# Optimization experiments

Measured on AMD Instinct MI355X. Metric: run time of the kernel, lower is better.

Reference implementation:

```python
import jax, jax.numpy as jnp
import numpy as np
from jax import lax

SIGMA = 1.0          # block_elemnts.combined_sigma
BN_EPS = 1e-5


def setup_inputs() -> dict:
    key = jax.random.key(0)
    k1, k2, k3, k4 = jax.random.split(key, 4)
    B, N, T, C_in, C_out = 8, 1024, 8, 64, 64
    return {
        "points": jax.random.normal(k1, (B, N, 3), dtype=jnp.float32),
        "translations": jax.random.normal(k2, (B, T, 3), dtype=jnp.float32),
        "functions": jax.random.normal(k3, (B, N, C_in), dtype=jnp.float32),
        "k_tensor": jax.random.normal(k4, (C_out, C_in, T), dtype=jnp.float32)
            * np.sqrt(2.0 / (C_in + C_out)),  # xavier_normal_
        "gamma": jnp.ones((C_out,), dtype=jnp.float32),
        "beta": jnp.zeros((C_out,), dtype=jnp.float32),
    }


def reference(points, translations, functions, k_tensor, gamma, beta):
    denom = 2.0 * SIGMA ** 2
    # pairwise squared distances [B,N,N]
    sq = jnp.sum(points * points, axis=-1)                      # [B,N]
    dist = sq[:, :, None] + sq[:, None, :] \
        - 2.0 * jnp.einsum('bnd,bmd->bnm', points, points)      # [B,N,N]
    # interpolation matrix = Gaussian kernel of distances
    interp_rowsum = jnp.sum(jnp.exp(-dist / denom), axis=2, keepdims=True)  # [B,N,1]
    w = functions / interp_rowsum                               # [B,N,Cin]
    # b_tensor[t] = w @ k_tensor[:,:,t]^T  -> [T,B,N,Cout]
    b = jnp.einsum('bnc,oct->tbno', w, k_tensor)
    ptd = jnp.einsum('bnd,btd->tbn', points, translations)      # [T,B,N]
    tsq = jnp.sum(translations * translations, axis=2).T        # [T,B]

    B_, N_, O_ = b.shape[1], b.shape[2], b.shape[3]

    def step(acc, inputs):
        b_t, ptd_t, tsq_t = inputs                              # [B,N,O],[B,N],[B]
        dot = -2.0 * ptd_t                                      # [B,N]
        # exponent = -||p_i - p_j - t||^2 / (2*sigma^2), always <= 0
        q = jnp.exp(-(dist + dot[:, :, None] - dot[:, None, :]
                      + tsq_t[:, None, None]) / denom)          # [B,N,N]
        return acc + jnp.einsum('bnm,bmo->bno', q, b_t), None

    out, _ = lax.scan(step, jnp.zeros((B_, N_, O_), dtype=b.dtype),
                      (b, ptd, tsq))                            # [B,N,O]

    # BatchNorm1d in training mode over (B,N) per channel, then ReLU
    mean = jnp.mean(out, axis=(0, 1))
    var = jnp.var(out, axis=(0, 1))
    xn = (out - mean) * lax.rsqrt(var + BN_EPS) * gamma + beta
    return jax.nn.relu(xn)                                      # [B,N,Cout]
```

## Files before the change

kernel.cpp:

```cpp
#include <hip/hip_runtime.h>
#include <hip/hip_bf16.h>
#include <cstdint>
#include <cstddef>

#define BN_EPS 1e-5f

typedef float f32x4_t __attribute__((ext_vector_type(4)));
typedef __bf16 bf16x8_t __attribute__((ext_vector_type(8)));

__device__ __forceinline__ unsigned short f2bf(float f) {
    __hip_bfloat16 h = __float2bfloat16(f);
    return __builtin_bit_cast(unsigned short, h);
}
__device__ __forceinline__ float bf2f(unsigned short u) {
    unsigned int v = ((unsigned int)u) << 16;
    return __builtin_bit_cast(float, v);
}

__device__ __forceinline__ void gld_lds16(void* lds, const void* gp) {
#if __has_builtin(__builtin_amdgcn_global_load_lds)
    __builtin_amdgcn_global_load_lds(
        (const __attribute__((address_space(1))) unsigned int*)gp,
        (__attribute__((address_space(3))) unsigned int*)lds, 16, 0, 0);
#else
    *(uint4*)lds = *(const uint4*)gp;
#endif
}


__global__ __launch_bounds__(256) void k_g(const float* __restrict__ points,
                                           const float* __restrict__ ktens,
                                           unsigned short* __restrict__ G,
                                           float* __restrict__ rowsum,
                                           unsigned short* __restrict__ kpb,
                                           float* __restrict__ bns) {
    __shared__ float praw[3072];
    __shared__ float px[1024], py[1024], pz[1024], hq[1024];
    __shared__ float part[8][128];
    __shared__ float p2[8][32];

    const int tid = threadIdx.x;
    if (blockIdx.x >= 1024) {
        const int i = (blockIdx.x - 1024) * 256 + tid;
        const int t = i >> 12, o = (i >> 6) & 63, c = i & 63;
        kpb[i] = f2bf(ktens[(o * 64 + c) * 8 + t]);
        if (blockIdx.x == 1024 && tid < 128) bns[tid] = 0.f;
        return;
    }

    const int b  = blockIdx.x & 7;
    const int n0 = (blockIdx.x >> 3) * 8;

    for (int i = tid; i < 3072; i += 256) praw[i] = points[b * 3072 + i];
    __syncthreads();
    for (int n = tid; n < 1024; n += 256) {
        float x = praw[n * 3], y = praw[n * 3 + 1], z = praw[n * 3 + 2];
        px[n] = x; py[n] = y; pz[n] = z;
        hq[n] = -0.5f * (x * x + y * y + z * z);
    }
    __syncthreads();

    const int rhalf = tid >> 7;
    const int c0 = (tid & 127) * 8;
    float vx[8], vy[8], vz[8], vh[8];
    *(float4*)&vx[0] = *(const float4*)&px[c0];
    *(float4*)&vx[4] = *(const float4*)&px[c0 + 4];
    *(float4*)&vy[0] = *(const float4*)&py[c0];
    *(float4*)&vy[4] = *(const float4*)&py[c0 + 4];
    *(float4*)&vz[0] = *(const float4*)&pz[c0];
    *(float4*)&vz[4] = *(const float4*)&pz[c0 + 4];
    *(float4*)&vh[0] = *(const float4*)&hq[c0];
    *(float4*)&vh[4] = *(const float4*)&hq[c0 + 4];

    unsigned short* gb = G + ((size_t)b << 20);

    #pragma unroll
    for (int u = 0; u < 4; ++u) {
        const int rl = u * 2 + rhalf;
        const int row = n0 + rl;
        const float rx = px[row], ry = py[row], rz = pz[row], hr = hq[row];
        unsigned short us[8];
        float ssum = 0.f;
        #pragma unroll
        for (int j = 0; j < 8; ++j) {
            float e = __expf(hr + vh[j] + rx * vx[j] + ry * vy[j] + rz * vz[j]);
            ssum += e;
            us[j] = f2bf(e);
        }
        uint4 pk;
        pk.x = us[0] | ((unsigned int)us[1] << 16);
        pk.y = us[2] | ((unsigned int)us[3] << 16);
        pk.z = us[4] | ((unsigned int)us[5] << 16);
        pk.w = us[6] | ((unsigned int)us[7] << 16);
        *(uint4*)(gb + (size_t)row * 1024 + c0) = pk;
        part[rl][tid & 127] = ssum;
    }
    __syncthreads();
    {
        const int row = tid >> 5, c4l = (tid & 31) * 4;
        float4 p = *(const float4*)&part[row][c4l];
        p2[row][tid & 31] = p.x + p.y + p.z + p.w;
    }
    __syncthreads();
    if (tid < 8) {
        float s = 0.f;
        #pragma unroll
        for (int q = 0; q < 8; ++q) {
            float4 v = *(const float4*)&p2[tid][q * 4];
            s += v.x + v.y + v.z + v.w;
        }
        rowsum[b * 1024 + n0 + tid] = s;
    }
}

__global__ __launch_bounds__(256) void k_prep(const float* __restrict__ points,
                                              const float* __restrict__ trans,
                                              const float* __restrict__ funcs,
                                              const unsigned short* __restrict__ kpb,
                                              const float* __restrict__ rowsum,
                                              unsigned short* __restrict__ bmatT,
                                              float* __restrict__ escale) {
    __shared__ unsigned short Asm[128 * 72];
    __shared__ unsigned short Bsm[128 * 72];
    __shared__ float sfacl[256];

    const int b  = blockIdx.x & 7;
    const int mt = (blockIdx.x >> 3) & 7;
    const int ct = blockIdx.x >> 6;
    const int m0 = mt * 128;

    const int tid  = threadIdx.x;
    const int wave = tid >> 6, lane = tid & 63;
    const int wr = wave >> 1, wc = wave & 1;
    const int fr = lane & 15, quad = lane >> 4;

    {
        const int tloc = tid >> 7, m = tid & 127;
        const int t = ct * 2 + tloc;
        const float tx = trans[b * 24 + t * 3], ty = trans[b * 24 + t * 3 + 1],
                    tz = trans[b * 24 + t * 3 + 2];
        const float* pp = &points[(size_t)(b * 1024 + m0 + m) * 3];
        const float ptd = pp[0] * tx + pp[1] * ty + pp[2] * tz;
        const float tsq = tx * tx + ty * ty + tz * tz;
        const float rsv = rowsum[b * 1024 + m0 + m];
        sfacl[tloc * 128 + m] = __expf(-ptd - 0.5f * tsq) / rsv;
        escale[(size_t)(b * 8 + t) * 1024 + m0 + m] = __expf(ptd);
    }
    #pragma unroll
    for (int rep = 0; rep < 2; ++rep) {
        const int m = rep * 64 + (tid >> 2);
        const int c16 = (tid & 3) * 16;
        const float* fp = &funcs[((size_t)(b * 1024) + m0 + m) * 64 + c16];
        float4 f0 = *(const float4*)fp, f1 = *(const float4*)(fp + 4);
        float4 f2 = *(const float4*)(fp + 8), f3 = *(const float4*)(fp + 12);
        uint4 p0, p1;
        p0.x = f2bf(f0.x) | ((unsigned)f2bf(f0.y) << 16);
        p0.y = f2bf(f0.z) | ((unsigned)f2bf(f0.w) << 16);
        p0.z = f2bf(f1.x) | ((unsigned)f2bf(f1.y) << 16);
        p0.w = f2bf(f1.z) | ((unsigned)f2bf(f1.w) << 16);
        p1.x = f2bf(f2.x) | ((unsigned)f2bf(f2.y) << 16);
        p1.y = f2bf(f2.z) | ((unsigned)f2bf(f2.w) << 16);
        p1.z = f2bf(f3.x) | ((unsigned)f2bf(f3.y) << 16);
        p1.w = f2bf(f3.z) | ((unsigned)f2bf(f3.w) << 16);
        *(uint4*)&Asm[m * 72 + c16] = p0;
        *(uint4*)&Asm[m * 72 + c16 + 8] = p1;
    }
    #pragma unroll
    for (int rep = 0; rep < 4; ++rep) {
        const int col = rep * 32 + (tid >> 3);
        const int c8 = (tid & 7) * 8;
        uint4 v = *(const uint4*)&kpb[(size_t)(ct * 128 + col) * 64 + c8];
        *(uint4*)&Bsm[col * 72 + c8] = v;
    }
    __syncthreads();

    f32x4_t acc[4][4];
    #pragma unroll
    for (int i = 0; i < 4; ++i)
        #pragma unroll
        for (int j = 0; j < 4; ++j) acc[i][j] = f32x4_t{0.f, 0.f, 0.f, 0.f};

    #pragma unroll
    for (int s = 0; s < 2; ++s) {
        uint4 afr[4], bfr[4];
        #pragma unroll
        for (int i = 0; i < 4; ++i)
            afr[i] = *(const uint4*)&Asm[(wr * 64 + i * 16 + fr) * 72 + s * 32 + quad * 8];
        #pragma unroll
        for (int j = 0; j < 4; ++j)
            bfr[j] = *(const uint4*)&Bsm[(wc * 64 + j * 16 + fr) * 72 + s * 32 + quad * 8];
        #pragma unroll
        for (int i = 0; i < 4; ++i)
            #pragma unroll
            for (int j = 0; j < 4; ++j)
                acc[i][j] = __builtin_amdgcn_mfma_f32_16x16x32_bf16(
                    __builtin_bit_cast(bf16x8_t, afr[i]),
                    __builtin_bit_cast(bf16x8_t, bfr[j]),
                    acc[i][j], 0, 0, 0);
    }

    #pragma unroll
    for (int i = 0; i < 4; ++i) {
        #pragma unroll
        for (int j = 0; j < 4; ++j) {
            const int colg = ct * 128 + wc * 64 + j * 16 + fr;
            ushort4 pk;
            {
                const int mb = wr * 64 + i * 16 + quad * 4;
                pk.x = f2bf(acc[i][j][0] * sfacl[wc * 128 + mb + 0]);
                pk.y = f2bf(acc[i][j][1] * sfacl[wc * 128 + mb + 1]);
                pk.z = f2bf(acc[i][j][2] * sfacl[wc * 128 + mb + 2]);
                pk.w = f2bf(acc[i][j][3] * sfacl[wc * 128 + mb + 3]);
                *(ushort4*)&bmatT[(size_t)(b * 512 + colg) * 1024 + m0 + mb] = pk;
            }
        }
    }
}

__global__ __launch_bounds__(256) void k_gemm(const unsigned short* __restrict__ G,
                                              const unsigned short* __restrict__ bmatT,
                                              const float* __restrict__ escale,
                                              unsigned short* __restrict__ He2) {
    __shared__ unsigned short As[4096];
    __shared__ unsigned short Bs[4096];
    __shared__ float escT[1024];

    const int b  = blockIdx.x & 7;
    const int rt = (blockIdx.x >> 3) & 7;
    const int z  = blockIdx.x >> 6;
    const int og = z & 3;
    const int kh = z >> 2;
    const int n0 = rt * 128;
    const int kb = kh * 256;

    const int tid  = threadIdx.x;
    const int wave = tid >> 6, lane = tid & 63;

    {
        const int t = tid >> 5, r4 = (tid & 31) * 4;
        *(float4*)&escT[t * 128 + r4] =
            *(const float4*)&escale[(size_t)(b * 8 + t) * 1024 + n0 + r4];
    }

    const unsigned short* gA = G + ((size_t)b << 20) + (size_t)n0 * 1024 + kb;
    const unsigned short* gB = bmatT + (size_t)(b * 512 + og * 16) * 1024 + kb;

    const int r16 = lane >> 2;
    const int kq  = lane & 3;
    const int gsw = kq ^ (r16 & 3);
    const size_t gAoff = (size_t)r16 * 1024 + gsw * 8;

    f32x4_t acc[2][8];
    #pragma unroll
    for (int i = 0; i < 2; ++i)
        #pragma unroll
        for (int j = 0; j < 8; ++j) acc[i][j] = f32x4_t{0.f, 0.f, 0.f, 0.f};

    const int fr = lane & 15;
    const int swoff = ((lane >> 4) ^ (fr & 3)) << 4;
    const int row_base = wave * 32;

    for (int kk = 0; kk < 8; ++kk) {
        const int k0 = kk * 32;
        __syncthreads();
        #pragma unroll
        for (int i = 0; i < 2; ++i) {
            const int seg = wave * 2 + i;
            gld_lds16((char*)As + seg * 1024 + lane * 16,
                      gA + (size_t)(seg * 16) * 1024 + k0 + gAoff);
            gld_lds16((char*)Bs + seg * 1024 + lane * 16,
                      gB + (size_t)(seg * 64) * 1024 + (size_t)r16 * 1024 + k0 + gsw * 8);
        }
        __syncthreads();
        uint4 afr0 = *(const uint4*)((const char*)As + (row_base + fr) * 64 + swoff);
        uint4 afr1 = *(const uint4*)((const char*)As + (row_base + 16 + fr) * 64 + swoff);
        #pragma unroll
        for (int j = 0; j < 8; ++j) {
            uint4 bfr = *(const uint4*)((const char*)Bs + (j * 16 + fr) * 64 + swoff);
            acc[0][j] = __builtin_amdgcn_mfma_f32_16x16x32_bf16(
                __builtin_bit_cast(bf16x8_t, afr0),
                __builtin_bit_cast(bf16x8_t, bfr), acc[0][j], 0, 0, 0);
            acc[1][j] = __builtin_amdgcn_mfma_f32_16x16x32_bf16(
                __builtin_bit_cast(bf16x8_t, afr1),
                __builtin_bit_cast(bf16x8_t, bfr), acc[1][j], 0, 0, 0);
        }
    }

    const int quad = lane >> 4, oo = lane & 15;
    unsigned short* dst = He2 + (size_t)kh * 524288
                              + (size_t)(b * 1024 + n0) * 64 + og * 16;
    #pragma unroll
    for (int i = 0; i < 2; ++i) {
        #pragma unroll
        for (int r = 0; r < 4; ++r) {
            const int row = row_base + i * 16 + quad * 4 + r;
            float s = 0.f;
            #pragma unroll
            for (int j = 0; j < 8; ++j)
                s += escT[j * 128 + row] * acc[i][j][r];
            dst[(size_t)row * 64 + oo] = f2bf(s);
        }
    }
}

__global__ __launch_bounds__(256) void k_fin(const unsigned short* __restrict__ He2,
                                             float* __restrict__ out,
                                             float* __restrict__ bns) {
    __shared__ float s1[16][64], s2[16][64];
    const int tid = threadIdx.x;
    float a0 = 0.f, a1 = 0.f, a2 = 0.f, a3 = 0.f;
    float q0 = 0.f, q1 = 0.f, q2 = 0.f, q3 = 0.f;
    #pragma unroll
    for (int it = 0; it < 2; ++it) {
        const size_t idx = (size_t)blockIdx.x * 512 + it * 256 + tid;
        float4 s = make_float4(0.f, 0.f, 0.f, 0.f);
        #pragma unroll
        for (int p = 0; p < 4; ++p) {
            ushort4 u = *(const ushort4*)(He2 + (size_t)p * 524288 + idx * 4);
            s.x += bf2f(u.x); s.y += bf2f(u.y); s.z += bf2f(u.z); s.w += bf2f(u.w);
        }
        ((float4*)out)[idx] = s;
        a0 += s.x; a1 += s.y; a2 += s.z; a3 += s.w;
        q0 += s.x * s.x; q1 += s.y * s.y; q2 += s.z * s.z; q3 += s.w * s.w;
    }
    const int g = tid >> 4, o4 = (tid & 15) * 4;
    *(float4*)&s1[g][o4] = make_float4(a0, a1, a2, a3);
    *(float4*)&s2[g][o4] = make_float4(q0, q1, q2, q3);
    __syncthreads();
    if (tid < 64) {
        float sa = 0.f, sb = 0.f;
        #pragma unroll
        for (int r = 0; r < 16; ++r) { sa += s1[r][tid]; sb += s2[r][tid]; }
        atomicAdd(&bns[tid], sa);
        atomicAdd(&bns[64 + tid], sb);
    }
}

__global__ __launch_bounds__(256) void k_bn(float* __restrict__ out,
                                            const float* __restrict__ bns,
                                            const float* __restrict__ gamma,
                                            const float* __restrict__ beta) {
    const int i = blockIdx.x * 256 + threadIdx.x;
    const int o4 = (i & 15) * 4;
    float4 x = ((float4*)out)[i];
    const float4 s  = *(const float4*)&bns[o4];
    const float4 s2 = *(const float4*)&bns[64 + o4];
    const float4 gm = *(const float4*)&gamma[o4];
    const float4 bt = *(const float4*)&beta[o4];
    const float invn = 1.f / 8192.f;
    float m, v, w;
    m = s.x * invn; v = s2.x * invn - m * m; w = __frsqrt_rn(v + BN_EPS) * gm.x;
    x.x = fmaxf((x.x - m) * w + bt.x, 0.f);
    m = s.y * invn; v = s2.y * invn - m * m; w = __frsqrt_rn(v + BN_EPS) * gm.y;
    x.y = fmaxf((x.y - m) * w + bt.y, 0.f);
    m = s.z * invn; v = s2.z * invn - m * m; w = __frsqrt_rn(v + BN_EPS) * gm.z;
    x.z = fmaxf((x.z - m) * w + bt.z, 0.f);
    m = s.w * invn; v = s2.w * invn - m * m; w = __frsqrt_rn(v + BN_EPS) * gm.w;
    x.w = fmaxf((x.w - m) * w + bt.w, 0.f);
    ((float4*)out)[i] = x;
}

extern "C" void kernel_launch(void* const* d_in, const int* in_sizes, int n_in,
                              void* d_out, int out_size, void* d_ws, size_t ws_size,
                              hipStream_t stream) {
    const float* points = (const float*)d_in[0];
    const float* trans  = (const float*)d_in[1];
    const float* funcs  = (const float*)d_in[2];
    const float* ktens  = (const float*)d_in[3];
    const float* gamma  = (const float*)d_in[4];
    const float* beta   = (const float*)d_in[5];
    float* out = (float*)d_out;

    float* ws      = (float*)d_ws;
    float* escale  = ws;
    float* bns     = escale + 65536;
    float* rowsum  = bns + 128;
    unsigned short* He2   = (unsigned short*)(rowsum + 8192);
    unsigned short* kpb   = He2 + 2097152;
    unsigned short* G     = kpb + 32768;
    unsigned short* bmatT = G + 8388608;

    k_g<<<1152, 256, 0, stream>>>(points, ktens, G, rowsum, kpb, bns);
    k_prep<<<256, 256, 0, stream>>>(points, trans, funcs, kpb, rowsum, bmatT, escale);
    k_gemm<<<1024, 256, 0, stream>>>(G, bmatT, escale, He2);
    k_fin<<<256, 256, 0, stream>>>(He2, out, bns);
    k_bn<<<512, 256, 0, stream>>>(out, bns, gamma, beta);
}
```

Measured before the change: 115.3 us.

## Recompute Gaussian matrix tiles inside GEMM instead of materializing G

The 16 MB bf16 Gaussian matrix G is no longer written by k_g. k_gemm now regenerates the A-operand fragments in registers from point coordinates staged in LDS, computing exp per element before each MFMA step. This removes the global write and re-read of G across the 4 output groups. The cost is more exp work, since each G tile is recomputed by every output-group and k-half block (4x redundancy), and those exps now sit on the MFMA critical path.

```diff
diff --git a/kernel.cpp b/kernel.cpp
--- a/kernel.cpp
+++ b/kernel.cpp
@@ -30,7 +30,6 @@
 
 __global__ __launch_bounds__(256) void k_g(const float* __restrict__ points,
                                            const float* __restrict__ ktens,
-                                           unsigned short* __restrict__ G,
                                            float* __restrict__ rowsum,
                                            unsigned short* __restrict__ kpb,
                                            float* __restrict__ bns) {
@@ -72,27 +71,15 @@
     *(float4*)&vh[0] = *(const float4*)&hq[c0];
     *(float4*)&vh[4] = *(const float4*)&hq[c0 + 4];
 
-    unsigned short* gb = G + ((size_t)b << 20);
-
     #pragma unroll
     for (int u = 0; u < 4; ++u) {
         const int rl = u * 2 + rhalf;
         const int row = n0 + rl;
         const float rx = px[row], ry = py[row], rz = pz[row], hr = hq[row];
-        unsigned short us[8];
         float ssum = 0.f;
         #pragma unroll
-        for (int j = 0; j < 8; ++j) {
-            float e = __expf(hr + vh[j] + rx * vx[j] + ry * vy[j] + rz * vz[j]);
-            ssum += e;
-            us[j] = f2bf(e);
-        }
-        uint4 pk;
-        pk.x = us[0] | ((unsigned int)us[1] << 16);
-        pk.y = us[2] | ((unsigned int)us[3] << 16);
-        pk.z = us[4] | ((unsigned int)us[5] << 16);
-        pk.w = us[6] | ((unsigned int)us[7] << 16);
-        *(uint4*)(gb + (size_t)row * 1024 + c0) = pk;
+        for (int j = 0; j < 8; ++j)
+            ssum += __expf(hr + vh[j] + rx * vx[j] + ry * vy[j] + rz * vz[j]);
         part[rl][tid & 127] = ssum;
     }
     __syncthreads();
@@ -217,13 +204,13 @@
     }
 }
 
-__global__ __launch_bounds__(256) void k_gemm(const unsigned short* __restrict__ G,
+__global__ __launch_bounds__(256) void k_gemm(const float* __restrict__ points,
                                               const unsigned short* __restrict__ bmatT,
                                               const float* __restrict__ escale,
                                               unsigned short* __restrict__ He2) {
-    __shared__ unsigned short As[4096];
     __shared__ unsigned short Bs[4096];
     __shared__ float escT[1024];
+    __shared__ float4 mp[256];
 
     const int b  = blockIdx.x & 7;
     const int rt = (blockIdx.x >> 3) & 7;
@@ -241,24 +228,38 @@
         *(float4*)&escT[t * 128 + r4] =
             *(const float4*)&escale[(size_t)(b * 8 + t) * 1024 + n0 + r4];
     }
-
-    const unsigned short* gA = G + ((size_t)b << 20) + (size_t)n0 * 1024 + kb;
+    {
+        const float* pp = &points[(size_t)(b * 1024 + kb + tid) * 3];
+        const float x = pp[0], y = pp[1], zz = pp[2];
+        mp[tid] = make_float4(x, y, zz, -0.5f * (x * x + y * y + zz * zz));
+    }
+
     const unsigned short* gB = bmatT + (size_t)(b * 512 + og * 16) * 1024 + kb;
 
     const int r16 = lane >> 2;
     const int kq  = lane & 3;
     const int gsw = kq ^ (r16 & 3);
-    const size_t gAoff = (size_t)r16 * 1024 + gsw * 8;
+
+    const int fr = lane & 15;
+    const int quad = lane >> 4;
+    const int swoff = (quad ^ (fr & 3)) << 4;
+    const int row_base = wave * 32;
+
+    float rx0, ry0, rz0, rh0, rx1, ry1, rz1, rh1;
+    {
+        const float* p0 = &points[(size_t)(b * 1024 + n0 + row_base + fr) * 3];
+        rx0 = p0[0]; ry0 = p0[1]; rz0 = p0[2];
+        rh0 = -0.5f * (rx0 * rx0 + ry0 * ry0 + rz0 * rz0);
+        const float* p1 = &points[(size_t)(b * 1024 + n0 + row_base + 16 + fr) * 3];
+        rx1 = p1[0]; ry1 = p1[1]; rz1 = p1[2];
+        rh1 = -0.5f * (rx1 * rx1 + ry1 * ry1 + rz1 * rz1);
+    }
 
     f32x4_t acc[2][8];
     #pragma unroll
     for (int i = 0; i < 2; ++i)
         #pragma unroll
         for (int j = 0; j < 8; ++j) acc[i][j] = f32x4_t{0.f, 0.f, 0.f, 0.f};
-
-    const int fr = lane & 15;
-    const int swoff = ((lane >> 4) ^ (fr & 3)) << 4;
-    const int row_base = wave * 32;
 
     for (int kk = 0; kk < 8; ++kk) {
         const int k0 = kk * 32;
@@ -266,14 +267,31 @@
         #pragma unroll
         for (int i = 0; i < 2; ++i) {
             const int seg = wave * 2 + i;
-            gld_lds16((char*)As + seg * 1024 + lane * 16,
-                      gA + (size_t)(seg * 16) * 1024 + k0 + gAoff);
             gld_lds16((char*)Bs + seg * 1024 + lane * 16,
                       gB + (size_t)(seg * 64) * 1024 + (size_t)r16 * 1024 + k0 + gsw * 8);
         }
+        uint4 afr0, afr1;
+        {
+            unsigned short u0[8], u1[8];
+            const int mbase = k0 + quad * 8;
+            #pragma unroll
+            for (int j = 0; j < 8; ++j) {
+                const float4 m4 = mp[mbase + j];
+                const float e0 = __expf(rh0 + m4.w + rx0 * m4.x + ry0 * m4.y + rz0 * m4.z);
+                const float e1 = __expf(rh1 + m4.w + rx1 * m4.x + ry1 * m4.y + rz1 * m4.z);
+                u0[j] = f2bf(e0);
+                u1[j] = f2bf(e1);
+            }
+            afr0.x = u0[0] | ((unsigned)u0[1] << 16);
+            afr0.y = u0[2] | ((unsigned)u0[3] << 16);
+            afr0.z = u0[4] | ((unsigned)u0[5] << 16);
+            afr0.w = u0[6] | ((unsigned)u0[7] << 16);
+            afr1.x = u1[0] | ((unsigned)u1[1] << 16);
+            afr1.y = u1[2] | ((unsigned)u1[3] << 16);
+            afr1.z = u1[4] | ((unsigned)u1[5] << 16);
+            afr1.w = u1[6] | ((unsigned)u1[7] << 16);
+        }
         __syncthreads();
-        uint4 afr0 = *(const uint4*)((const char*)As + (row_base + fr) * 64 + swoff);
-        uint4 afr1 = *(const uint4*)((const char*)As + (row_base + 16 + fr) * 64 + swoff);
         #pragma unroll
         for (int j = 0; j < 8; ++j) {
             uint4 bfr = *(const uint4*)((const char*)Bs + (j * 16 + fr) * 64 + swoff);
@@ -286,7 +304,7 @@
         }
     }
 
-    const int quad = lane >> 4, oo = lane & 15;
+    const int oo = lane & 15;
     unsigned short* dst = He2 + (size_t)kh * 524288
                               + (size_t)(b * 1024 + n0) * 64 + og * 16;
     #pragma unroll
@@ -377,12 +395,11 @@
     float* rowsum  = bns + 128;
     unsigned short* He2   = (unsigned short*)(rowsum + 8192);
     unsigned short* kpb   = He2 + 2097152;
-    unsigned short* G     = kpb + 32768;
-    unsigned short* bmatT = G + 8388608;
-
-    k_g<<<1152, 256, 0, stream>>>(points, ktens, G, rowsum, kpb, bns);
+    unsigned short* bmatT = kpb + 32768;
+
+    k_g<<<1152, 256, 0, stream>>>(points, ktens, rowsum, kpb, bns);
     k_prep<<<256, 256, 0, stream>>>(points, trans, funcs, kpb, rowsum, bmatT, escale);
-    k_gemm<<<1024, 256, 0, stream>>>(G, bmatT, escale, He2);
+    k_gemm<<<1024, 256, 0, stream>>>(points, bmatT, escale, He2);
     k_fin<<<256, 256, 0, stream>>>(He2, out, bns);
     k_bn<<<512, 256, 0, stream>>>(out, bns, gamma, beta);
 }
```

New measurement: 112.4 us. 1.03x faster.
